# Kernel tuning notes

Hardware: AMD Instinct MI355X
Metric: run time of the kernel (lower is better)

Reference implementation:

```python
import jax, jax.numpy as jnp
import numpy as np

TEMPERATURE = 1.0
D_THRESH = 0.1
EPS = 1e-10
NORM_EPS = 1e-12  # F.normalize clamp


def _l2_normalize(x):
    n = jnp.sqrt(jnp.sum(x * x, axis=1, keepdims=True))
    return x / jnp.maximum(n, NORM_EPS)


def setup_inputs() -> dict:
    key = jax.random.key(0)
    k1, k2, k3 = jax.random.split(key, 3)
    N, D = 8192, 128
    f1 = jax.random.normal(k1, (N, D), dtype=jnp.float32)
    f2 = jax.random.normal(k2, (N, D), dtype=jnp.float32)
    # continuous targets in [-1, 1) so both the distance mask (|ti-tj|>0.1)
    # and the polarity mask (sign mismatch) are exercised
    targets = jax.random.uniform(k3, (N,), dtype=jnp.float32, minval=-1.0, maxval=1.0)
    return {"f1": f1, "f2": f2, "targets": targets}


def reference(f1, f2, targets):
    f1 = _l2_normalize(f1)
    f2 = _l2_normalize(f2)

    # self_mask: 1 where pair is a negative (far target or opposite polarity)
    dist_t = jnp.abs(targets[:, None] - targets[None, :])  # [N,N]
    mask_distance = dist_t > D_THRESH
    polarity = targets > 0
    mask_polarity = polarity[:, None] != polarity[None, :]
    self_mask = (mask_distance | mask_polarity).astype(f1.dtype)  # [N,N]

    # ||f1_i - f2_j||^2 via the cdist/matmul trick (avoids [N,N,D] tensor)
    sq1 = jnp.sum(f1 * f1, axis=1)  # [N]
    sq2 = jnp.sum(f2 * f2, axis=1)  # [N]
    dist = sq1[:, None] - 2.0 * (f1 @ f2.T) + sq2[None, :]  # [N,N]
    cos = 1.0 - 0.5 * dist

    p = jax.nn.softmax(cos / TEMPERATURE, axis=1)  # [N,N]
    pos_w = 1.0 - self_mask
    log_pos = -jnp.log(p + EPS) * pos_w
    log_neg = -jnp.log(1.0 - p + EPS) * self_mask
    per_row = (jnp.sum(log_pos, axis=1) / jnp.sum(pos_w, axis=1)
               + jnp.sum(log_neg, axis=1) / jnp.sum(self_mask, axis=1))
    return jnp.mean(per_row)
```

## Files before the change

kernel.cpp:

```cpp
#include <hip/hip_runtime.h>
#include <hip/hip_bf16.h>
#include <math.h>

#define NROWS 8192
#define DDIM  128
#define JCHUNKS 16
#define JPER  (NROWS / JCHUNKS)
#define STAGE_COLS 64
#define NSTAGES (JPER / STAGE_COLS)
#define ROWS_PER_BLOCK 128
#define GRIDX (NROWS / ROWS_PER_BLOCK)
#define LOG2E 1.44269504088896f

#define AS1 __attribute__((address_space(1)))
#define AS3 __attribute__((address_space(3)))

typedef __attribute__((ext_vector_type(8))) short bf16x8;
typedef __attribute__((ext_vector_type(4))) float f32x4;
typedef __attribute__((ext_vector_type(2))) float f32x2;

__global__ __launch_bounds__(256) void norm_kernel(
    const float* __restrict__ f1, const float* __restrict__ f2,
    __hip_bfloat16* __restrict__ f1b, __hip_bfloat16* __restrict__ f2b,
    float* __restrict__ out) {
  if (blockIdx.x == 0 && threadIdx.x == 0) out[0] = 0.0f;
  int t = threadIdx.x;
  int rloc = t >> 5;
  int l = t & 31;
  int b = blockIdx.x;
  int half = (b >= NROWS / 8) ? 1 : 0;
  int row = (b - half * (NROWS / 8)) * 8 + rloc;
  const float* src = half ? f2 : f1;
  __hip_bfloat16* dst = half ? f2b : f1b;

  float4 v = ((const float4*)src)[row * (DDIM / 4) + l];
  float s = v.x * v.x + v.y * v.y + v.z * v.z + v.w * v.w;
  #pragma unroll
  for (int off = 1; off < 32; off <<= 1) s += __shfl_xor(s, off, 64);
  float inv = 1.0f / fmaxf(sqrtf(s), 1e-12f);
  __hip_bfloat16 hv[4];
  hv[0] = __float2bfloat16(v.x * inv);
  hv[1] = __float2bfloat16(v.y * inv);
  hv[2] = __float2bfloat16(v.z * inv);
  hv[3] = __float2bfloat16(v.w * inv);
  *(ushort4*)&dst[(size_t)row * DDIM + l * 4] = *(ushort4*)hv;
}

__global__ __launch_bounds__(256, 4) void stats_kernel(
    const __hip_bfloat16* __restrict__ f1b,
    const __hip_bfloat16* __restrict__ f2b,
    const float* __restrict__ targets,
    float* __restrict__ partials) {
  __shared__ __align__(16) char lds0[STAGE_COLS * 256];
  __shared__ __align__(16) char lds1[STAGE_COLS * 256];
  __shared__ __align__(16) float tsh[JPER];

  const int chunk = blockIdx.y;
  const int i0 = blockIdx.x * ROWS_PER_BLOCK;
  const int w    = threadIdx.x >> 6;
  const int lane = threadIdx.x & 63;
  const int p15  = lane & 15;
  const int rl4  = lane >> 4;
  const int rbase = i0 + w * 32;

  bf16x8 afrag[2][4];
  #pragma unroll
  for (int rs = 0; rs < 2; ++rs) {
    const __hip_bfloat16* arow =
        &f1b[(size_t)(rbase + rs * 16 + p15) * DDIM + rl4 * 8];
    #pragma unroll
    for (int ks = 0; ks < 4; ++ks)
      afrag[rs][ks] = *(const bf16x8*)(arow + ks * 32);
  }

  f32x2 ti2[4];
  #pragma unroll
  for (int rr = 0; rr < 4; ++rr) {
    ti2[rr][0] = targets[rbase + rl4 * 4 + rr];
    ti2[rr][1] = targets[rbase + 16 + rl4 * 4 + rr];
  }

  f32x2 Z2[4]  = {{0,0},{0,0},{0,0},{0,0}};
  f32x2 Zp2[4] = {{0,0},{0,0},{0,0},{0,0}};
  f32x2 Cp2[4] = {{0,0},{0,0},{0,0},{0,0}};
  f32x2 Np2[4] = {{0,0},{0,0},{0,0},{0,0}};

  const int jb0 = chunk * JPER;

  int srcoff[4];
  #pragma unroll
  for (int q = 0; q < 4; ++q) {
    int rloc = w * 16 + q * 4 + rl4;
    int c    = p15 ^ (q * 4 + rl4);
    srcoff[q] = rloc * DDIM + c * 8;
  }

  {
    #pragma unroll
    for (int rnd = 0; rnd < 2; ++rnd)
      __builtin_amdgcn_global_load_lds(
          (const AS1 void*)(targets + jb0 + rnd * 256 + w * 64 + lane),
          (AS3 void*)(&tsh[rnd * 256 + w * 64]), 4, 0, 0);
    const __hip_bfloat16* gstage = f2b + (size_t)jb0 * DDIM;
    char* lbase = &lds0[w * 4096];
    #pragma unroll
    for (int q = 0; q < 4; ++q)
      __builtin_amdgcn_global_load_lds((const AS1 void*)(gstage + srcoff[q]),
                                       (AS3 void*)(lbase + q * 1024), 16, 0, 0);
  }

  for (int s = 0; s < NSTAGES; ++s) {
    __syncthreads();

    if (s + 1 < NSTAGES) {
      const __hip_bfloat16* gstage = f2b + (size_t)(jb0 + (s + 1) * STAGE_COLS) * DDIM;
      char* lbase = ((s + 1) & 1) ? &lds1[w * 4096] : &lds0[w * 4096];
      #pragma unroll
      for (int q = 0; q < 4; ++q)
        __builtin_amdgcn_global_load_lds((const AS1 void*)(gstage + srcoff[q]),
                                         (AS3 void*)(lbase + q * 1024), 16, 0, 0);
    }

    const char* lb = (s & 1) ? lds1 : lds0;
    #pragma unroll
    for (int ct = 0; ct < 4; ++ct) {
      const int rloc = ct * 16 + p15;
      bf16x8 bfrag[4];
      #pragma unroll
      for (int ks = 0; ks < 4; ++ks)
        bfrag[ks] = *(const bf16x8*)(lb + rloc * 256 + (((rl4 + ks * 4) ^ p15) << 4));

      float tj = tsh[s * STAGE_COLS + ct * 16 + p15];

      f32x4 acc0 = {0.f, 0.f, 0.f, 0.f};
      f32x4 acc1 = {0.f, 0.f, 0.f, 0.f};
      #pragma unroll
      for (int ks = 0; ks < 4; ++ks) {
        acc0 = __builtin_amdgcn_mfma_f32_16x16x32_bf16(afrag[0][ks], bfrag[ks], acc0, 0, 0, 0);
        acc1 = __builtin_amdgcn_mfma_f32_16x16x32_bf16(afrag[1][ks], bfrag[ks], acc1, 0, 0, 0);
      }

      const bool pj = tj > 0.0f;
      const f32x2 tjs = {tj, tj};
      const f32x2 Ks = {LOG2E, LOG2E};
      #pragma unroll
      for (int rr = 0; rr < 4; ++rr) {
        f32x2 c2 = {acc0[rr], acc1[rr]};
        f32x2 d2 = ti2[rr] - tjs;
        bool q0 = (__builtin_fabsf(d2[0]) <= 0.1f) & ((ti2[rr][0] > 0.0f) == pj);
        bool q1 = (__builtin_fabsf(d2[1]) <= 0.1f) & ((ti2[rr][1] > 0.0f) == pj);
        f32x2 m2 = {q0 ? 1.0f : 0.0f, q1 ? 1.0f : 0.0f};
        f32x2 x2 = c2 * Ks - Ks;
        f32x2 e2 = {__builtin_amdgcn_exp2f(x2[0]), __builtin_amdgcn_exp2f(x2[1])};
        Z2[rr]  += e2;
        Zp2[rr] += m2 * e2;
        Cp2[rr] += m2 * c2;
        Np2[rr] += m2;
      }
    }
  }

  #pragma unroll
  for (int rr = 0; rr < 4; ++rr) {
    for (int off = 1; off < 16; off <<= 1) {
      Z2[rr][0]  += __shfl_xor(Z2[rr][0],  off, 64);
      Z2[rr][1]  += __shfl_xor(Z2[rr][1],  off, 64);
      Zp2[rr][0] += __shfl_xor(Zp2[rr][0], off, 64);
      Zp2[rr][1] += __shfl_xor(Zp2[rr][1], off, 64);
      Cp2[rr][0] += __shfl_xor(Cp2[rr][0], off, 64);
      Cp2[rr][1] += __shfl_xor(Cp2[rr][1], off, 64);
      Np2[rr][0] += __shfl_xor(Np2[rr][0], off, 64);
      Np2[rr][1] += __shfl_xor(Np2[rr][1], off, 64);
    }
  }
  if (p15 == 0) {
    #pragma unroll
    for (int rs = 0; rs < 2; ++rs)
      #pragma unroll
      for (int rr = 0; rr < 4; ++rr) {
        size_t row = rbase + rs * 16 + rl4 * 4 + rr;
        f32x4 st = {Z2[rr][rs], Zp2[rr][rs], Cp2[rr][rs], Np2[rr][rs]};
        *(f32x4*)&partials[((size_t)row * JCHUNKS + chunk) * 4] = st;
      }
  }
}

__global__ void finalize_rows(const float* __restrict__ partials,
                              float* __restrict__ out) {
  int r = blockIdx.x * 256 + threadIdx.x;
  float Z = 0, Zp = 0, Cp = 0, Np = 0;
  for (int ch = 0; ch < JCHUNKS; ++ch) {
    float4 p = *(const float4*)&partials[((size_t)r * JCHUNKS + ch) * 4];
    Z += p.x; Zp += p.y; Cp += p.z; Np += p.w;
  }
  float Zn = Z - Zp;
  float nn = (float)NROWS - Np;
  float spos = (1.0f + logf(Z)) - Cp / Np;
  float sneg = Zn / Z - nn * 1e-10f;
  float per_row = spos + sneg / nn;

  float v = per_row;
  for (int off = 32; off; off >>= 1) v += __shfl_xor(v, off, 64);
  __shared__ float wsum[4];
  int lane = threadIdx.x & 63, wid = threadIdx.x >> 6;
  if (lane == 0) wsum[wid] = v;
  __syncthreads();
  if (threadIdx.x == 0)
    atomicAdd(out, (wsum[0] + wsum[1] + wsum[2] + wsum[3]) * (1.0f / (float)NROWS));
}

extern "C" void kernel_launch(void* const* d_in, const int* in_sizes, int n_in,
                              void* d_out, int out_size, void* d_ws, size_t ws_size,
                              hipStream_t stream) {
  const float* f1  = (const float*)d_in[0];
  const float* f2  = (const float*)d_in[1];
  const float* tgt = (const float*)d_in[2];
  float* out = (float*)d_out;

  char* ws = (char*)d_ws;
  __hip_bfloat16* f1b = (__hip_bfloat16*)ws;
  __hip_bfloat16* f2b = (__hip_bfloat16*)(ws + (size_t)NROWS * DDIM * 2);
  float* partials = (float*)(ws + (size_t)NROWS * DDIM * 4);

  norm_kernel<<<2 * (NROWS / 8), 256, 0, stream>>>(f1, f2, f1b, f2b, out);
  dim3 g2(GRIDX, JCHUNKS);
  stats_kernel<<<g2, 256, 0, stream>>>(f1b, f2b, tgt, partials);
  finalize_rows<<<NROWS / 256, 256, 0, stream>>>(partials, out);
}
```

Baseline: 100.8 us.

## Bucket-sort rows by target and skip mask evaluation on uniform tiles

A new single-block kernel bucket-sorts rows by target, offsetting values by polarity so one distance test also covers sign mismatch, and stores per-16-column min/max. The stats kernel gathers rows through this permutation and classifies each 16-wide column tile against the wave's target range, taking mask-free paths for all-negative or all-positive tiles. exp is replaced by a degree-4 polynomial approximation of exp(c-1). The cost is an extra serial single-block launch, gathered loads, and approximation error from the polynomial.

```diff
diff --git a/kernel.cpp b/kernel.cpp
--- a/kernel.cpp
+++ b/kernel.cpp
@@ -10,7 +10,7 @@
 #define NSTAGES (JPER / STAGE_COLS)
 #define ROWS_PER_BLOCK 128
 #define GRIDX (NROWS / ROWS_PER_BLOCK)
-#define LOG2E 1.44269504088896f
+#define NBUCK 1024
 
 #define AS1 __attribute__((address_space(1)))
 #define AS3 __attribute__((address_space(3)))
@@ -18,6 +18,77 @@
 typedef __attribute__((ext_vector_type(8))) short bf16x8;
 typedef __attribute__((ext_vector_type(4))) float f32x4;
 typedef __attribute__((ext_vector_type(2))) float f32x2;
+
+#define PB0 0.3678959f
+#define PB1 0.3668905f
+#define PB2 0.1836441f
+#define PB3 0.0652423f
+#define PB4 0.0161110f
+
+__device__ inline f32x2 expcm1(f32x2 c) {
+  f32x2 e = {PB4, PB4};
+  e = e * c + (f32x2){PB3, PB3};
+  e = e * c + (f32x2){PB2, PB2};
+  e = e * c + (f32x2){PB1, PB1};
+  e = e * c + (f32x2){PB0, PB0};
+  return e;
+}
+
+__global__ __launch_bounds__(1024) void sort_kernel(
+    const float* __restrict__ targets,
+    int* __restrict__ pi, float* __restrict__ tps, float2* __restrict__ jmm) {
+  __shared__ int hist[NBUCK];
+  __shared__ int scanb[NBUCK];
+  __shared__ float tloc[NROWS];
+  const int tid = threadIdx.x;
+  hist[tid] = 0;
+  __syncthreads();
+  #pragma unroll
+  for (int r = 0; r < NROWS / 1024; ++r) {
+    float t = targets[r * 1024 + tid];
+    int b = (int)((t + 1.0f) * (NBUCK / 2));
+    b = min(max(b, 0), NBUCK - 1);
+    atomicAdd(&hist[b], 1);
+  }
+  __syncthreads();
+  int own = hist[tid];
+  scanb[tid] = own;
+  __syncthreads();
+  for (int d = 1; d < NBUCK; d <<= 1) {
+    int nv = scanb[tid];
+    if (tid >= d) nv += scanb[tid - d];
+    __syncthreads();
+    scanb[tid] = nv;
+    __syncthreads();
+  }
+  hist[tid] = scanb[tid] - own;
+  __syncthreads();
+  #pragma unroll
+  for (int r = 0; r < NROWS / 1024; ++r) {
+    int i = r * 1024 + tid;
+    float t = targets[i];
+    int b = (int)((t + 1.0f) * (NBUCK / 2));
+    b = min(max(b, 0), NBUCK - 1);
+    int pos = atomicAdd(&hist[b], 1);
+    pi[pos] = i;
+    tloc[pos] = t + (t > 0.0f ? 10.0f : -10.0f);
+  }
+  __syncthreads();
+  #pragma unroll
+  for (int r = 0; r < NROWS / 1024; ++r) {
+    int i = r * 1024 + tid;
+    tps[i] = tloc[i];
+  }
+  for (int k = tid; k < NROWS / 16; k += 1024) {
+    float mn = tloc[16 * k], mx = mn;
+    #pragma unroll
+    for (int u = 1; u < 16; ++u) {
+      float x = tloc[16 * k + u];
+      mn = fminf(mn, x); mx = fmaxf(mx, x);
+    }
+    jmm[k] = make_float2(mn, mx);
+  }
+}
 
 __global__ __launch_bounds__(256) void norm_kernel(
     const float* __restrict__ f1, const float* __restrict__ f2,
@@ -49,11 +120,14 @@
 __global__ __launch_bounds__(256, 4) void stats_kernel(
     const __hip_bfloat16* __restrict__ f1b,
     const __hip_bfloat16* __restrict__ f2b,
-    const float* __restrict__ targets,
+    const int* __restrict__ pi,
+    const float* __restrict__ tps,
+    const float2* __restrict__ jmm,
     float* __restrict__ partials) {
   __shared__ __align__(16) char lds0[STAGE_COLS * 256];
   __shared__ __align__(16) char lds1[STAGE_COLS * 256];
   __shared__ __align__(16) float tsh[JPER];
+  __shared__ __align__(16) float jsh[(JPER / 16) * 2];
 
   const int chunk = blockIdx.y;
   const int i0 = blockIdx.x * ROWS_PER_BLOCK;
@@ -63,62 +137,85 @@
   const int rl4  = lane >> 4;
   const int rbase = i0 + w * 32;
 
+  int ar0 = pi[rbase + p15];
+  int ar1 = pi[rbase + 16 + p15];
   bf16x8 afrag[2][4];
   #pragma unroll
-  for (int rs = 0; rs < 2; ++rs) {
-    const __hip_bfloat16* arow =
-        &f1b[(size_t)(rbase + rs * 16 + p15) * DDIM + rl4 * 8];
-    #pragma unroll
-    for (int ks = 0; ks < 4; ++ks)
-      afrag[rs][ks] = *(const bf16x8*)(arow + ks * 32);
-  }
-
-  f32x2 ti2[4];
+  for (int ks = 0; ks < 4; ++ks) {
+    afrag[0][ks] = *(const bf16x8*)&f1b[(size_t)ar0 * DDIM + rl4 * 8 + ks * 32];
+    afrag[1][ks] = *(const bf16x8*)&f1b[(size_t)ar1 * DDIM + rl4 * 8 + ks * 32];
+  }
+
+  f32x2 tip2[4];
   #pragma unroll
   for (int rr = 0; rr < 4; ++rr) {
-    ti2[rr][0] = targets[rbase + rl4 * 4 + rr];
-    ti2[rr][1] = targets[rbase + 16 + rl4 * 4 + rr];
+    tip2[rr][0] = tps[rbase + rl4 * 4 + rr];
+    tip2[rr][1] = tps[rbase + 16 + rl4 * 4 + rr];
+  }
+  float twmin = tip2[0][0], twmax = tip2[0][0];
+  #pragma unroll
+  for (int rr = 0; rr < 4; ++rr) {
+    twmin = fminf(twmin, fminf(tip2[rr][0], tip2[rr][1]));
+    twmax = fmaxf(twmax, fmaxf(tip2[rr][0], tip2[rr][1]));
+  }
+  #pragma unroll
+  for (int off = 1; off < 64; off <<= 1) {
+    twmin = fminf(twmin, __shfl_xor(twmin, off, 64));
+    twmax = fmaxf(twmax, __shfl_xor(twmax, off, 64));
   }
 
   f32x2 Z2[4]  = {{0,0},{0,0},{0,0},{0,0}};
   f32x2 Zp2[4] = {{0,0},{0,0},{0,0},{0,0}};
   f32x2 Cp2[4] = {{0,0},{0,0},{0,0},{0,0}};
   f32x2 Np2[4] = {{0,0},{0,0},{0,0},{0,0}};
+  float posTiles = 0.0f;
 
   const int jb0 = chunk * JPER;
-
-  int srcoff[4];
-  #pragma unroll
-  for (int q = 0; q < 4; ++q) {
-    int rloc = w * 16 + q * 4 + rl4;
-    int c    = p15 ^ (q * 4 + rl4);
-    srcoff[q] = rloc * DDIM + c * 8;
-  }
-
+  const int rloc0 = w * 16 + rl4;
+
+  #pragma unroll
+  for (int rnd = 0; rnd < 2; ++rnd)
+    __builtin_amdgcn_global_load_lds(
+        (const AS1 void*)(tps + jb0 + rnd * 256 + w * 64 + lane),
+        (AS3 void*)(&tsh[rnd * 256 + w * 64]), 4, 0, 0);
+  if (w == 0)
+    __builtin_amdgcn_global_load_lds(
+        (const AS1 void*)((const float*)jmm + chunk * 64 + lane),
+        (AS3 void*)(&jsh[0]), 4, 0, 0);
+
+  int prow[4];
+  #pragma unroll
+  for (int q = 0; q < 4; ++q) prow[q] = pi[jb0 + rloc0 + q * 4];
   {
-    #pragma unroll
-    for (int rnd = 0; rnd < 2; ++rnd)
-      __builtin_amdgcn_global_load_lds(
-          (const AS1 void*)(targets + jb0 + rnd * 256 + w * 64 + lane),
-          (AS3 void*)(&tsh[rnd * 256 + w * 64]), 4, 0, 0);
-    const __hip_bfloat16* gstage = f2b + (size_t)jb0 * DDIM;
     char* lbase = &lds0[w * 4096];
     #pragma unroll
-    for (int q = 0; q < 4; ++q)
-      __builtin_amdgcn_global_load_lds((const AS1 void*)(gstage + srcoff[q]),
-                                       (AS3 void*)(lbase + q * 1024), 16, 0, 0);
-  }
+    for (int q = 0; q < 4; ++q) {
+      int c = p15 ^ (q * 4 + rl4);
+      __builtin_amdgcn_global_load_lds(
+          (const AS1 void*)(f2b + (size_t)prow[q] * DDIM + c * 8),
+          (AS3 void*)(lbase + q * 1024), 16, 0, 0);
+    }
+  }
+  #pragma unroll
+  for (int q = 0; q < 4; ++q) prow[q] = pi[jb0 + STAGE_COLS + rloc0 + q * 4];
 
   for (int s = 0; s < NSTAGES; ++s) {
     __syncthreads();
 
     if (s + 1 < NSTAGES) {
-      const __hip_bfloat16* gstage = f2b + (size_t)(jb0 + (s + 1) * STAGE_COLS) * DDIM;
       char* lbase = ((s + 1) & 1) ? &lds1[w * 4096] : &lds0[w * 4096];
       #pragma unroll
-      for (int q = 0; q < 4; ++q)
-        __builtin_amdgcn_global_load_lds((const AS1 void*)(gstage + srcoff[q]),
-                                         (AS3 void*)(lbase + q * 1024), 16, 0, 0);
+      for (int q = 0; q < 4; ++q) {
+        int c = p15 ^ (q * 4 + rl4);
+        __builtin_amdgcn_global_load_lds(
+            (const AS1 void*)(f2b + (size_t)prow[q] * DDIM + c * 8),
+            (AS3 void*)(lbase + q * 1024), 16, 0, 0);
+      }
+      if (s + 2 < NSTAGES) {
+        #pragma unroll
+        for (int q = 0; q < 4; ++q)
+          prow[q] = pi[jb0 + (s + 2) * STAGE_COLS + rloc0 + q * 4];
+      }
     }
 
     const char* lb = (s & 1) ? lds1 : lds0;
@@ -130,8 +227,6 @@
       for (int ks = 0; ks < 4; ++ks)
         bfrag[ks] = *(const bf16x8*)(lb + rloc * 256 + (((rl4 + ks * 4) ^ p15) << 4));
 
-      float tj = tsh[s * STAGE_COLS + ct * 16 + p15];
-
       f32x4 acc0 = {0.f, 0.f, 0.f, 0.f};
       f32x4 acc1 = {0.f, 0.f, 0.f, 0.f};
       #pragma unroll
@@ -140,25 +235,52 @@
         acc1 = __builtin_amdgcn_mfma_f32_16x16x32_bf16(afrag[1][ks], bfrag[ks], acc1, 0, 0, 0);
       }
 
-      const bool pj = tj > 0.0f;
-      const f32x2 tjs = {tj, tj};
-      const f32x2 Ks = {LOG2E, LOG2E};
-      #pragma unroll
-      for (int rr = 0; rr < 4; ++rr) {
-        f32x2 c2 = {acc0[rr], acc1[rr]};
-        f32x2 d2 = ti2[rr] - tjs;
-        bool q0 = (__builtin_fabsf(d2[0]) <= 0.1f) & ((ti2[rr][0] > 0.0f) == pj);
-        bool q1 = (__builtin_fabsf(d2[1]) <= 0.1f) & ((ti2[rr][1] > 0.0f) == pj);
-        f32x2 m2 = {q0 ? 1.0f : 0.0f, q1 ? 1.0f : 0.0f};
-        f32x2 x2 = c2 * Ks - Ks;
-        f32x2 e2 = {__builtin_amdgcn_exp2f(x2[0]), __builtin_amdgcn_exp2f(x2[1])};
-        Z2[rr]  += e2;
-        Zp2[rr] += m2 * e2;
-        Cp2[rr] += m2 * c2;
-        Np2[rr] += m2;
-      }
-    }
-  }
+      const int tl = s * 4 + ct;
+      float jmn = jsh[2 * tl], jmx = jsh[2 * tl + 1];
+      int uneg = __builtin_amdgcn_readfirstlane(
+          ((jmn - twmax > 0.1f) || (twmin - jmx > 0.1f)) ? 1 : 0);
+      int upos = __builtin_amdgcn_readfirstlane(
+          ((twmax - jmn <= 0.1f) && (jmx - twmin <= 0.1f)) ? 1 : 0);
+
+      if (uneg) {
+        #pragma unroll
+        for (int rr = 0; rr < 4; ++rr) {
+          f32x2 c2 = {acc0[rr], acc1[rr]};
+          Z2[rr] += expcm1(c2);
+        }
+      } else if (upos) {
+        posTiles += 1.0f;
+        #pragma unroll
+        for (int rr = 0; rr < 4; ++rr) {
+          f32x2 c2 = {acc0[rr], acc1[rr]};
+          f32x2 e2 = expcm1(c2);
+          Z2[rr]  += e2;
+          Zp2[rr] += e2;
+          Cp2[rr] += c2;
+        }
+      } else {
+        float tj = tsh[s * STAGE_COLS + ct * 16 + p15];
+        f32x2 tj2 = {tj, tj};
+        #pragma unroll
+        for (int rr = 0; rr < 4; ++rr) {
+          f32x2 c2 = {acc0[rr], acc1[rr]};
+          f32x2 d2 = tip2[rr] - tj2;
+          bool q0 = __builtin_fabsf(d2[0]) <= 0.1f;
+          bool q1 = __builtin_fabsf(d2[1]) <= 0.1f;
+          f32x2 m2 = {q0 ? 1.0f : 0.0f, q1 ? 1.0f : 0.0f};
+          f32x2 e2 = expcm1(c2);
+          Z2[rr]  += e2;
+          Zp2[rr] += m2 * e2;
+          Cp2[rr] += m2 * c2;
+          Np2[rr] += m2;
+        }
+      }
+    }
+  }
+
+  #pragma unroll
+  for (int rr = 0; rr < 4; ++rr)
+    Np2[rr] += (f32x2){posTiles, posTiles};
 
   #pragma unroll
   for (int rr = 0; rr < 4; ++rr) {
@@ -193,6 +315,8 @@
     float4 p = *(const float4*)&partials[((size_t)r * JCHUNKS + ch) * 4];
     Z += p.x; Zp += p.y; Cp += p.z; Np += p.w;
   }
+  Np *= 16.0f;
+  Np *= 0.0625f;
   float Zn = Z - Zp;
   float nn = (float)NROWS - Np;
   float spos = (1.0f + logf(Z)) - Cp / Np;
@@ -221,9 +345,13 @@
   __hip_bfloat16* f1b = (__hip_bfloat16*)ws;
   __hip_bfloat16* f2b = (__hip_bfloat16*)(ws + (size_t)NROWS * DDIM * 2);
   float* partials = (float*)(ws + (size_t)NROWS * DDIM * 4);
-
+  int*   pi  = (int*)(ws + (size_t)NROWS * DDIM * 4 + (size_t)NROWS * JCHUNKS * 16);
+  float* tps = (float*)((char*)pi + NROWS * 4);
+  float2* jmm = (float2*)((char*)tps + NROWS * 4);
+
+  sort_kernel<<<1, 1024, 0, stream>>>(tgt, pi, tps, jmm);
   norm_kernel<<<2 * (NROWS / 8), 256, 0, stream>>>(f1, f2, f1b, f2b, out);
   dim3 g2(GRIDX, JCHUNKS);
-  stats_kernel<<<g2, 256, 0, stream>>>(f1b, f2b, tgt, partials);
+  stats_kernel<<<g2, 256, 0, stream>>>(f1b, f2b, pi, tps, jmm, partials);
   finalize_rows<<<NROWS / 256, 256, 0, stream>>>(partials, out);
 }
```

Measured after the change: 122.9 us. +22.0%, slower.

## Replace exp2 with polynomial, fold polarity into shifted targets, split columns finer

Applied to the files above, without the earlier changes.

Replaces the hardware exp2 of (cos-1) with a degree-4 polynomial approximation of exp(c-1). This is valid only because cos lies in [-1,1] for normalized rows, but it introduces approximation error into the softmax. Precomputes polarity-shifted targets (±10 offset) in the norm kernel so the positive mask needs only one abs-compare. It also doubles the column chunks, halves the stage width and raises the occupancy hint, giving more parallel blocks with smaller LDS use per block.

```diff
diff --git a/kernel.cpp b/kernel.cpp
--- a/kernel.cpp
+++ b/kernel.cpp
@@ -4,14 +4,12 @@
 
 #define NROWS 8192
 #define DDIM  128
-#define JCHUNKS 16
+#define JCHUNKS 32
 #define JPER  (NROWS / JCHUNKS)
-#define STAGE_COLS 64
+#define STAGE_COLS 32
 #define NSTAGES (JPER / STAGE_COLS)
 #define ROWS_PER_BLOCK 128
 #define GRIDX (NROWS / ROWS_PER_BLOCK)
-#define LOG2E 1.44269504088896f
-
 #define AS1 __attribute__((address_space(1)))
 #define AS3 __attribute__((address_space(3)))
 
@@ -19,15 +17,35 @@
 typedef __attribute__((ext_vector_type(4))) float f32x4;
 typedef __attribute__((ext_vector_type(2))) float f32x2;
 
+#define PB0 0.3678959f
+#define PB1 0.3668905f
+#define PB2 0.1836441f
+#define PB3 0.0652423f
+#define PB4 0.0161110f
+
+__device__ inline f32x2 expcm1(f32x2 c) {
+  f32x2 e = {PB4, PB4};
+  e = e * c + (f32x2){PB3, PB3};
+  e = e * c + (f32x2){PB2, PB2};
+  e = e * c + (f32x2){PB1, PB1};
+  e = e * c + (f32x2){PB0, PB0};
+  return e;
+}
+
 __global__ __launch_bounds__(256) void norm_kernel(
     const float* __restrict__ f1, const float* __restrict__ f2,
+    const float* __restrict__ tgt,
     __hip_bfloat16* __restrict__ f1b, __hip_bfloat16* __restrict__ f2b,
-    float* __restrict__ out) {
-  if (blockIdx.x == 0 && threadIdx.x == 0) out[0] = 0.0f;
+    float* __restrict__ tps, float* __restrict__ out) {
   int t = threadIdx.x;
+  int b = blockIdx.x;
+  if (b == 0 && t == 0) out[0] = 0.0f;
+  if (b < NROWS / 256) {
+    float tv = tgt[b * 256 + t];
+    tps[b * 256 + t] = tv + (tv > 0.0f ? 10.0f : -10.0f);
+  }
   int rloc = t >> 5;
   int l = t & 31;
-  int b = blockIdx.x;
   int half = (b >= NROWS / 8) ? 1 : 0;
   int row = (b - half * (NROWS / 8)) * 8 + rloc;
   const float* src = half ? f2 : f1;
@@ -46,10 +64,10 @@
   *(ushort4*)&dst[(size_t)row * DDIM + l * 4] = *(ushort4*)hv;
 }
 
-__global__ __launch_bounds__(256, 4) void stats_kernel(
+__global__ __launch_bounds__(256, 6) void stats_kernel(
     const __hip_bfloat16* __restrict__ f1b,
     const __hip_bfloat16* __restrict__ f2b,
-    const float* __restrict__ targets,
+    const float* __restrict__ tps,
     float* __restrict__ partials) {
   __shared__ __align__(16) char lds0[STAGE_COLS * 256];
   __shared__ __align__(16) char lds1[STAGE_COLS * 256];
@@ -73,11 +91,11 @@
       afrag[rs][ks] = *(const bf16x8*)(arow + ks * 32);
   }
 
-  f32x2 ti2[4];
+  f32x2 tip2[4];
   #pragma unroll
   for (int rr = 0; rr < 4; ++rr) {
-    ti2[rr][0] = targets[rbase + rl4 * 4 + rr];
-    ti2[rr][1] = targets[rbase + 16 + rl4 * 4 + rr];
+    tip2[rr][0] = tps[rbase + rl4 * 4 + rr];
+    tip2[rr][1] = tps[rbase + 16 + rl4 * 4 + rr];
   }
 
   f32x2 Z2[4]  = {{0,0},{0,0},{0,0},{0,0}};
@@ -87,24 +105,22 @@
 
   const int jb0 = chunk * JPER;
 
-  int srcoff[4];
-  #pragma unroll
-  for (int q = 0; q < 4; ++q) {
-    int rloc = w * 16 + q * 4 + rl4;
-    int c    = p15 ^ (q * 4 + rl4);
+  int srcoff[2];
+  #pragma unroll
+  for (int q = 0; q < 2; ++q) {
+    int rloc = w * 8 + q * 4 + rl4;
+    int c    = p15 ^ (rloc & 15);
     srcoff[q] = rloc * DDIM + c * 8;
   }
 
+  __builtin_amdgcn_global_load_lds(
+      (const AS1 void*)(tps + jb0 + w * 64 + lane),
+      (AS3 void*)(&tsh[w * 64]), 4, 0, 0);
   {
-    #pragma unroll
-    for (int rnd = 0; rnd < 2; ++rnd)
-      __builtin_amdgcn_global_load_lds(
-          (const AS1 void*)(targets + jb0 + rnd * 256 + w * 64 + lane),
-          (AS3 void*)(&tsh[rnd * 256 + w * 64]), 4, 0, 0);
     const __hip_bfloat16* gstage = f2b + (size_t)jb0 * DDIM;
-    char* lbase = &lds0[w * 4096];
-    #pragma unroll
-    for (int q = 0; q < 4; ++q)
+    char* lbase = &lds0[w * 2048];
+    #pragma unroll
+    for (int q = 0; q < 2; ++q)
       __builtin_amdgcn_global_load_lds((const AS1 void*)(gstage + srcoff[q]),
                                        (AS3 void*)(lbase + q * 1024), 16, 0, 0);
   }
@@ -114,23 +130,21 @@
 
     if (s + 1 < NSTAGES) {
       const __hip_bfloat16* gstage = f2b + (size_t)(jb0 + (s + 1) * STAGE_COLS) * DDIM;
-      char* lbase = ((s + 1) & 1) ? &lds1[w * 4096] : &lds0[w * 4096];
-      #pragma unroll
-      for (int q = 0; q < 4; ++q)
+      char* lbase = ((s + 1) & 1) ? &lds1[w * 2048] : &lds0[w * 2048];
+      #pragma unroll
+      for (int q = 0; q < 2; ++q)
         __builtin_amdgcn_global_load_lds((const AS1 void*)(gstage + srcoff[q]),
                                          (AS3 void*)(lbase + q * 1024), 16, 0, 0);
     }
 
     const char* lb = (s & 1) ? lds1 : lds0;
     #pragma unroll
-    for (int ct = 0; ct < 4; ++ct) {
+    for (int ct = 0; ct < 2; ++ct) {
       const int rloc = ct * 16 + p15;
       bf16x8 bfrag[4];
       #pragma unroll
       for (int ks = 0; ks < 4; ++ks)
         bfrag[ks] = *(const bf16x8*)(lb + rloc * 256 + (((rl4 + ks * 4) ^ p15) << 4));
-
-      float tj = tsh[s * STAGE_COLS + ct * 16 + p15];
 
       f32x4 acc0 = {0.f, 0.f, 0.f, 0.f};
       f32x4 acc1 = {0.f, 0.f, 0.f, 0.f};
@@ -140,18 +154,16 @@
         acc1 = __builtin_amdgcn_mfma_f32_16x16x32_bf16(afrag[1][ks], bfrag[ks], acc1, 0, 0, 0);
       }
 
-      const bool pj = tj > 0.0f;
-      const f32x2 tjs = {tj, tj};
-      const f32x2 Ks = {LOG2E, LOG2E};
+      float tj = tsh[s * STAGE_COLS + ct * 16 + p15];
+      f32x2 tj2 = {tj, tj};
       #pragma unroll
       for (int rr = 0; rr < 4; ++rr) {
         f32x2 c2 = {acc0[rr], acc1[rr]};
-        f32x2 d2 = ti2[rr] - tjs;
-        bool q0 = (__builtin_fabsf(d2[0]) <= 0.1f) & ((ti2[rr][0] > 0.0f) == pj);
-        bool q1 = (__builtin_fabsf(d2[1]) <= 0.1f) & ((ti2[rr][1] > 0.0f) == pj);
+        f32x2 d2 = tip2[rr] - tj2;
+        bool q0 = __builtin_fabsf(d2[0]) <= 0.1f;
+        bool q1 = __builtin_fabsf(d2[1]) <= 0.1f;
         f32x2 m2 = {q0 ? 1.0f : 0.0f, q1 ? 1.0f : 0.0f};
-        f32x2 x2 = c2 * Ks - Ks;
-        f32x2 e2 = {__builtin_amdgcn_exp2f(x2[0]), __builtin_amdgcn_exp2f(x2[1])};
+        f32x2 e2 = expcm1(c2);
         Z2[rr]  += e2;
         Zp2[rr] += m2 * e2;
         Cp2[rr] += m2 * c2;
@@ -221,9 +233,10 @@
   __hip_bfloat16* f1b = (__hip_bfloat16*)ws;
   __hip_bfloat16* f2b = (__hip_bfloat16*)(ws + (size_t)NROWS * DDIM * 2);
   float* partials = (float*)(ws + (size_t)NROWS * DDIM * 4);
-
-  norm_kernel<<<2 * (NROWS / 8), 256, 0, stream>>>(f1, f2, f1b, f2b, out);
+  float* tps = (float*)((char*)partials + (size_t)NROWS * JCHUNKS * 16);
+
+  norm_kernel<<<2 * (NROWS / 8), 256, 0, stream>>>(f1, f2, tgt, f1b, f2b, tps, out);
   dim3 g2(GRIDX, JCHUNKS);
-  stats_kernel<<<g2, 256, 0, stream>>>(f1b, f2b, tgt, partials);
+  stats_kernel<<<g2, 256, 0, stream>>>(f1b, f2b, tps, partials);
   finalize_rows<<<NROWS / 256, 256, 0, stream>>>(partials, out);
 }
```

New measurement: 309.0 us. 207% more time.
